# Optimization experiments

Measured on AMD Instinct MI355X. Metric: run time of the kernel, lower is better.

The kernel has to match this reference:

```python
import jax, jax.numpy as jnp
import numpy as np

DIM = 1024
NUM_EXPERTS = 8
TOP_K = 2


def setup_inputs() -> dict:
    key = jax.random.key(0)
    ks = jax.random.split(key, 7)
    s_in = 1.0 / np.sqrt(DIM)
    s_hid = 1.0 / np.sqrt(4 * DIM)
    x = jax.random.normal(ks[0], (2, 2048, DIM), dtype=jnp.float32)
    gate_w = jax.random.normal(ks[1], (DIM, NUM_EXPERTS), dtype=jnp.float32) * s_in
    gate_b = jax.random.normal(ks[2], (NUM_EXPERTS,), dtype=jnp.float32) * 0.01
    w1 = jax.random.normal(ks[3], (NUM_EXPERTS, DIM, 4 * DIM), dtype=jnp.float32) * s_in
    b1 = jax.random.normal(ks[4], (NUM_EXPERTS, 4 * DIM), dtype=jnp.float32) * 0.01
    w2 = jax.random.normal(ks[5], (NUM_EXPERTS, 4 * DIM, DIM), dtype=jnp.float32) * s_hid
    b2 = jax.random.normal(ks[6], (NUM_EXPERTS, DIM), dtype=jnp.float32) * 0.01
    return {"x": x, "gate_w": gate_w, "gate_b": gate_b, "w1": w1, "b1": b1, "w2": w2, "b2": b2}


def reference(x, gate_w, gate_b, w1, b1, w2, b2):
    # Faithful to the torch module in EVAL mode (no routing noise).
    # Quirks reproduced: (1) gather of expert inputs degenerates to flat_x
    # (all top_k copies identical); (2) softmax-normalized gates are dead code
    # (never applied); (3) the per-expert masked assignment overwrites all
    # TOP_K. Net: out = TOP_K * FFN_{max(topk_idx)}(x).
    B, N, C = x.shape
    flat_x = x.reshape(-1, C)                      # [T, C]
    logits = flat_x @ gate_w + gate_b              # [T, E]
    _, topk_idx = jax.lax.top_k(logits, TOP_K)     # [T, k]
    e_star = jnp.max(topk_idx, axis=-1)            # [T] last-overwriting expert
    out = jnp.zeros_like(flat_x)
    for i in range(NUM_EXPERTS):                   # fixed small expert loop
        h = jax.nn.gelu(flat_x @ w1[i] + b1[i], approximate=False)  # exact GELU (torch default)
        y = h @ w2[i] + b2[i]                      # [T, C]
        out = jnp.where((e_star == i)[:, None], y, out)
    return (TOP_K * out).reshape(B, N, C)
```

## Files before the change

kernel.cpp:

```cpp
#include <hip/hip_runtime.h>
#include <hip/hip_bf16.h>
#include <hip/hip_fp16.h>

#define T_TOKENS 4096
#define DIMC 1024
#define HID 4096
#define NE 8

typedef _Float16 f16;
typedef _Float16 f16x8 __attribute__((ext_vector_type(8)));
typedef _Float16 f16x4 __attribute__((ext_vector_type(4)));
typedef float f32x4 __attribute__((ext_vector_type(4)));

__device__ __forceinline__ void gload_lds16(const f16* g, f16* l) {
    __builtin_amdgcn_global_load_lds(
        (const __attribute__((address_space(1))) void*)g,
        (__attribute__((address_space(3))) void*)l, 16, 0, 0);
}

__global__ __launch_bounds__(256) void gating_kernel(
    const float* __restrict__ x, const float* __restrict__ gw,
    const float* __restrict__ gb, int* __restrict__ counts,
    int* __restrict__ list)
{
    const int wave = threadIdx.x >> 6;
    const int lane = threadIdx.x & 63;
    const int t = blockIdx.x * 4 + wave;

    const float* xr = x + (size_t)t * DIMC;
    float acc[NE];
#pragma unroll
    for (int e = 0; e < NE; ++e) acc[e] = 0.f;

    for (int i = 0; i < DIMC / 64; ++i) {
        const int k = i * 64 + lane;
        const float xv = xr[k];
        const float* g = gw + (size_t)k * NE;
#pragma unroll
        for (int e = 0; e < NE; ++e) acc[e] = fmaf(xv, g[e], acc[e]);
    }
#pragma unroll
    for (int off = 32; off >= 1; off >>= 1) {
#pragma unroll
        for (int e = 0; e < NE; ++e) acc[e] += __shfl_xor(acc[e], off, 64);
    }
    if (lane == 0) {
        float lg[NE];
#pragma unroll
        for (int e = 0; e < NE; ++e) lg[e] = acc[e] + gb[e];
        int i1 = 0; float v1 = lg[0];
#pragma unroll
        for (int e = 1; e < NE; ++e) { if (lg[e] > v1) { v1 = lg[e]; i1 = e; } }
        int i2 = -1; float v2 = -3.4e38f;
#pragma unroll
        for (int e = 0; e < NE; ++e) {
            if (e == i1) continue;
            if (lg[e] > v2) { v2 = lg[e]; i2 = e; }
        }
        const int es = (i1 > i2) ? i1 : i2;
        const int pos = atomicAdd(&counts[es], 1);
        list[es * T_TOKENS + pos] = t;
    }
}

__global__ __launch_bounds__(256) void xconvert(const float* __restrict__ x,
                                                f16* __restrict__ xh)
{
    const size_t i = ((size_t)blockIdx.x * 256 + threadIdx.x) * 8;
    const float4 a = *(const float4*)(x + i);
    const float4 b = *(const float4*)(x + i + 4);
    f16x8 v;
    v[0] = (f16)a.x; v[1] = (f16)a.y; v[2] = (f16)a.z; v[3] = (f16)a.w;
    v[4] = (f16)b.x; v[5] = (f16)b.y; v[6] = (f16)b.z; v[7] = (f16)b.w;
    *(f16x8*)(xh + i) = v;
}

__global__ __launch_bounds__(256) void wconvert(const float* __restrict__ W,
                                                f16* __restrict__ Wt,
                                                int K, int N)
{
    __shared__ f16 Lt[64 * 72];
    const int n0 = blockIdx.x * 64;
    const int k0 = blockIdx.y * 64;
    const float* Ws = W + (size_t)blockIdx.z * K * N;
    const int t = threadIdx.x;

    const int no = (t & 15) * 4;
    const int kr = t >> 4;
#pragma unroll
    for (int p = 0; p < 4; ++p) {
        const int k = kr + p * 16;
        const float4 v = *(const float4*)(Ws + (size_t)(k0 + k) * N + n0 + no);
        Lt[(no + 0) * 72 + k] = (f16)v.x;
        Lt[(no + 1) * 72 + k] = (f16)v.y;
        Lt[(no + 2) * 72 + k] = (f16)v.z;
        Lt[(no + 3) * 72 + k] = (f16)v.w;
    }
    __syncthreads();
    const int n = t >> 2;
    const int ko = (t & 3) * 16;
    const f16x8 a = *(const f16x8*)&Lt[n * 72 + ko];
    const f16x8 b = *(const f16x8*)&Lt[n * 72 + ko + 8];
    f16* dst = Wt + ((size_t)blockIdx.z * N + n0 + n) * K + k0 + ko;
    *(f16x8*)(dst) = a;
    *(f16x8*)(dst + 8) = b;
}

template <bool FIRST>
__global__ __launch_bounds__(512) void ffn_gemm5(
    const f16* __restrict__ A, const f16* __restrict__ Bt,
    const float* __restrict__ bias, const int* __restrict__ counts,
    const int* __restrict__ list, f16* __restrict__ Hout,
    float* __restrict__ pout)
{
    constexpr int KB   = FIRST ? DIMC : HID;
    constexpr int NTOT = FIRST ? HID : DIMC;

    const int e   = FIRST ? (int)blockIdx.z : (int)(blockIdx.z >> 2);
    const int ks  = FIRST ? 0 : (int)(blockIdx.z & 3);
    const int kk0 = ks * 1024;
    const int m0  = blockIdx.y * 256;
    const int n0  = blockIdx.x * 128;
    const int cnt = counts[e];
    if (m0 >= cnt) return;

    __shared__ __align__(16) f16 As[3][256 * 64];
    __shared__ __align__(16) f16 Bs[3][128 * 64];
    __shared__ int rows[256];

    const int tid = threadIdx.x;
    if (tid < 256) rows[tid] = (m0 + tid < cnt) ? list[e * T_TOKENS + m0 + tid] : -1;
    __syncthreads();

    const int lane = tid & 63;
    const int wv   = tid >> 6;
    const int wr   = wv >> 1;
    const int wc   = wv & 1;

    const f16* asrc[4];
    const f16* bsrc[2];
#pragma unroll
    for (int j = 0; j < 4; ++j) {
        const int row   = wv * 32 + j * 8 + (lane >> 3);
        const int chunk = (lane & 7) ^ (row & 7);
        int tok = rows[row]; if (tok < 0) tok = 0;
        asrc[j] = A + (size_t)tok * KB + kk0 + chunk * 8;
    }
#pragma unroll
    for (int j = 0; j < 2; ++j) {
        const int row   = wv * 16 + j * 8 + (lane >> 3);
        const int chunk = (lane & 7) ^ (row & 7);
        bsrc[j] = Bt + ((size_t)e * NTOT + n0 + row) * KB + kk0 + chunk * 8;
    }

    f32x4 acc[4][4];
#pragma unroll
    for (int mi = 0; mi < 4; ++mi)
#pragma unroll
        for (int ni = 0; ni < 4; ++ni) acc[mi][ni] = f32x4{0.f, 0.f, 0.f, 0.f};

#define STG(BUF, KT)                                                          \
    do {                                                                      \
        _Pragma("unroll")                                                     \
        for (int j = 0; j < 4; ++j)                                           \
            gload_lds16(asrc[j] + (KT) * 64, &As[BUF][(wv * 32 + j * 8) * 64]); \
        _Pragma("unroll")                                                     \
        for (int j = 0; j < 2; ++j)                                           \
            gload_lds16(bsrc[j] + (KT) * 64, &Bs[BUF][(wv * 16 + j * 8) * 64]); \
    } while (0)

#define CMP(BUF)                                                              \
    do {                                                                      \
        _Pragma("unroll")                                                     \
        for (int kh = 0; kh < 2; ++kh) {                                      \
            f16x8 af[4], bf[4];                                               \
            _Pragma("unroll")                                                 \
            for (int mi = 0; mi < 4; ++mi) {                                  \
                const int row = wr * 64 + mi * 16 + (lane & 15);              \
                const int kb  = (((lane >> 4) * 16) + kh * 64) ^ ((row & 7) << 4); \
                af[mi] = *(const f16x8*)((const char*)As[BUF] + row * 128 + kb);   \
            }                                                                 \
            _Pragma("unroll")                                                 \
            for (int ni = 0; ni < 4; ++ni) {                                  \
                const int n  = wc * 64 + ni * 16 + (lane & 15);               \
                const int kb = (((lane >> 4) * 16) + kh * 64) ^ ((n & 7) << 4);    \
                bf[ni] = *(const f16x8*)((const char*)Bs[BUF] + n * 128 + kb);     \
            }                                                                 \
            _Pragma("unroll")                                                 \
            for (int mi = 0; mi < 4; ++mi)                                    \
                _Pragma("unroll")                                             \
                for (int ni = 0; ni < 4; ++ni)                                \
                    acc[mi][ni] = __builtin_amdgcn_mfma_f32_16x16x32_f16(     \
                        af[mi], bf[ni], acc[mi][ni], 0, 0, 0);                \
        }                                                                     \
    } while (0)

    STG(0, 0);
    STG(1, 1);
#pragma unroll
    for (int kt = 0; kt < 16; ++kt) {
        if (kt + 2 < 16) STG((kt + 2) % 3, kt + 2);
        if (kt < 14)       asm volatile("s_waitcnt vmcnt(12)" ::: "memory");
        else if (kt == 14) asm volatile("s_waitcnt vmcnt(6)"  ::: "memory");
        else               asm volatile("s_waitcnt vmcnt(0)"  ::: "memory");
        __builtin_amdgcn_s_barrier();
        __builtin_amdgcn_sched_barrier(0);
        CMP(kt % 3);
        __builtin_amdgcn_s_barrier();
        __builtin_amdgcn_sched_barrier(0);
    }
#undef STG
#undef CMP

#pragma unroll
    for (int ni = 0; ni < 4; ++ni) {
        const int gc = n0 + wc * 64 + ni * 16 + (lane & 15);
        const float bv = FIRST ? bias[(size_t)e * HID + gc]
                               : ((ks == 0) ? 2.f * bias[(size_t)e * DIMC + gc] : 0.f);
#pragma unroll
        for (int mi = 0; mi < 4; ++mi) {
#pragma unroll
            for (int r = 0; r < 4; ++r) {
                const int lrow = wr * 64 + mi * 16 + (lane >> 4) * 4 + r;
                const int tok = rows[lrow];
                if (tok < 0) continue;
                if (FIRST) {
                    const float v = acc[mi][ni][r] + bv;
                    const float g = 0.5f * v * (1.f + erff(v * 0.70710678118f));
                    Hout[(size_t)tok * HID + gc] = (f16)g;
                } else {
                    pout[((size_t)ks * T_TOKENS + tok) * DIMC + gc] =
                        2.f * acc[mi][ni][r] + bv;
                }
            }
        }
    }
}

__global__ __launch_bounds__(256) void reduce4(const float* __restrict__ p,
                                               float* __restrict__ out)
{
    constexpr size_t SL = (size_t)T_TOKENS * DIMC;
    const size_t i = ((size_t)blockIdx.x * 256 + threadIdx.x) * 4;
    const float4 a = *(const float4*)(p + i);
    const float4 b = *(const float4*)(p + SL + i);
    const float4 c = *(const float4*)(p + 2 * SL + i);
    const float4 d = *(const float4*)(p + 3 * SL + i);
    float4 s;
    s.x = a.x + b.x + c.x + d.x;
    s.y = a.y + b.y + c.y + d.y;
    s.z = a.z + b.z + c.z + d.z;
    s.w = a.w + b.w + c.w + d.w;
    *(float4*)(out + i) = s;
}

template <bool FIRST>
__global__ __launch_bounds__(256) void ffn_gemm3(
    const f16* __restrict__ A, const f16* __restrict__ Bt,
    const float* __restrict__ bias, const int* __restrict__ counts,
    const int* __restrict__ list, f16* __restrict__ Hout,
    float* __restrict__ out)
{
    constexpr int KB   = FIRST ? DIMC : HID;
    constexpr int NTOT = FIRST ? HID : DIMC;
    constexpr int NKT  = 16;

    const int e   = FIRST ? (int)blockIdx.z : (int)(blockIdx.z >> 2);
    const int ks  = FIRST ? 0 : (int)(blockIdx.z & 3);
    const int kk0 = ks * 1024;
    const int m0  = blockIdx.y * 128;
    const int n0  = blockIdx.x * 128;
    const int cnt = counts[e];
    if (m0 >= cnt) return;

    __shared__ __align__(16) f16 As[128 * 64];
    __shared__ __align__(16) f16 Bs[128 * 64];
    __shared__ int rows[128];

    const int tid = threadIdx.x;
    if (tid < 128) rows[tid] = (m0 + tid < cnt) ? list[e * T_TOKENS + m0 + tid] : -1;
    __syncthreads();

    const int lane = tid & 63;
    const int wv   = tid >> 6;
    const int wr   = wv >> 1, wc = wv & 1;

    const f16* asrc[4];
    const f16* bsrc[4];
    f16* adst[4];
    f16* bdst[4];
#pragma unroll
    for (int j = 0; j < 4; ++j) {
        const int row   = wv * 32 + j * 8 + (lane >> 3);
        const int chunk = (lane & 7) ^ (row & 7);
        int tok = rows[row]; if (tok < 0) tok = 0;
        asrc[j] = A + (size_t)tok * KB + kk0 + chunk * 8;
        bsrc[j] = Bt + ((size_t)e * NTOT + n0 + row) * KB + kk0 + chunk * 8;
        adst[j] = As + (wv * 32 + j * 8) * 64;
        bdst[j] = Bs + (wv * 32 + j * 8) * 64;
    }

    f32x4 acc[4][4];
#pragma unroll
    for (int mi = 0; mi < 4; ++mi)
#pragma unroll
        for (int ni = 0; ni < 4; ++ni) acc[mi][ni] = f32x4{0.f, 0.f, 0.f, 0.f};

    for (int kt = 0; kt < NKT; ++kt) {
        const int ko = kt * 64;
        __syncthreads();
#pragma unroll
        for (int j = 0; j < 4; ++j) {
            gload_lds16(asrc[j] + ko, adst[j]);
            gload_lds16(bsrc[j] + ko, bdst[j]);
        }
        __syncthreads();
#pragma unroll
        for (int kh = 0; kh < 2; ++kh) {
            f16x8 af[4], bf[4];
#pragma unroll
            for (int mi = 0; mi < 4; ++mi) {
                const int row = wr * 64 + mi * 16 + (lane & 15);
                const int kb  = (((lane >> 4) * 16) + kh * 64) ^ ((row & 7) << 4);
                af[mi] = *(const f16x8*)((const char*)As + row * 128 + kb);
            }
#pragma unroll
            for (int ni = 0; ni < 4; ++ni) {
                const int n  = wc * 64 + ni * 16 + (lane & 15);
                const int kb = (((lane >> 4) * 16) + kh * 64) ^ ((n & 7) << 4);
                bf[ni] = *(const f16x8*)((const char*)Bs + n * 128 + kb);
            }
#pragma unroll
            for (int mi = 0; mi < 4; ++mi)
#pragma unroll
                for (int ni = 0; ni < 4; ++ni)
                    acc[mi][ni] = __builtin_amdgcn_mfma_f32_16x16x32_f16(
                        af[mi], bf[ni], acc[mi][ni], 0, 0, 0);
        }
    }

#pragma unroll
    for (int ni = 0; ni < 4; ++ni) {
        const int gc = n0 + wc * 64 + ni * 16 + (lane & 15);
        const float bv = FIRST ? bias[(size_t)e * HID + gc]
                               : ((ks == 0) ? 2.f * bias[(size_t)e * DIMC + gc] : 0.f);
#pragma unroll
        for (int mi = 0; mi < 4; ++mi) {
#pragma unroll
            for (int r = 0; r < 4; ++r) {
                const int lrow = wr * 64 + mi * 16 + (lane >> 4) * 4 + r;
                const int tok = rows[lrow];
                if (tok < 0) continue;
                if (FIRST) {
                    const float v = acc[mi][ni][r] + bv;
                    const float g = 0.5f * v * (1.f + erff(v * 0.70710678118f));
                    Hout[(size_t)tok * HID + gc] = (f16)g;
                } else {
                    atomicAdd(out + (size_t)tok * DIMC + gc,
                              2.f * acc[mi][ni][r] + bv);
                }
            }
        }
    }
}

template <bool FIRST>
__global__ __launch_bounds__(256) void ffn_gemm_fb(
    const float* __restrict__ x, const f16* __restrict__ Hin,
    const float* __restrict__ w1, const float* __restrict__ b1,
    const float* __restrict__ w2, const float* __restrict__ b2,
    const int* __restrict__ counts, const int* __restrict__ list,
    f16* __restrict__ Hout, float* __restrict__ out)
{
    constexpr int K = FIRST ? DIMC : HID;
    constexpr int N = FIRST ? HID : DIMC;
    constexpr int LDT = 40;

    const int e  = blockIdx.z;
    const int m0 = blockIdx.y * 128;
    const int n0 = blockIdx.x * 128;
    const int cnt = counts[e];
    if (m0 >= cnt) return;

    __shared__ f16 Ab[128 * LDT];
    __shared__ f16 Bb[128 * LDT];
    __shared__ int rows[128];

    const int tid = threadIdx.x;
    if (tid < 128) {
        const int p = m0 + tid;
        rows[tid] = (p < cnt) ? list[e * T_TOKENS + p] : -1;
    }
    __syncthreads();

    const int lane = tid & 63;
    const int wv = tid >> 6;
    const int wr = wv >> 1, wc = wv & 1;

    f32x4 acc[4][4];
#pragma unroll
    for (int mi = 0; mi < 4; ++mi)
#pragma unroll
        for (int ni = 0; ni < 4; ++ni) acc[mi][ni] = f32x4{0.f, 0.f, 0.f, 0.f};

    const float* Bsrc = (FIRST ? w1 : w2) + (size_t)e * K * N;

    for (int kk = 0; kk < K; kk += 32) {
        __syncthreads();
        {
            const int r  = tid >> 3;
            const int ko = (tid & 7) * 4;
#pragma unroll
            for (int p = 0; p < 4; ++p) {
                const int row = p * 32 + r;
                const int tok = rows[row];
                f16x4 hv;
                if (FIRST) {
                    float4 v;
                    if (tok >= 0) v = *(const float4*)(x + (size_t)tok * K + kk + ko);
                    else          v = make_float4(0.f, 0.f, 0.f, 0.f);
                    hv[0] = (f16)v.x; hv[1] = (f16)v.y; hv[2] = (f16)v.z; hv[3] = (f16)v.w;
                } else {
                    if (tok >= 0) hv = *(const f16x4*)(Hin + (size_t)tok * K + kk + ko);
                    else { hv[0] = (f16)0.f; hv[1] = (f16)0.f; hv[2] = (f16)0.f; hv[3] = (f16)0.f; }
                }
                *(f16x4*)&Ab[row * LDT + ko] = hv;
            }
        }
        {
            const int kb = tid >> 5;
            const int no = (tid & 31) * 4;
#pragma unroll
            for (int p = 0; p < 4; ++p) {
                const int k = p * 8 + kb;
                const float4 v = *(const float4*)(Bsrc + (size_t)(kk + k) * N + n0 + no);
                f16 h[4];
                h[0] = (f16)v.x; h[1] = (f16)v.y; h[2] = (f16)v.z; h[3] = (f16)v.w;
#pragma unroll
                for (int i = 0; i < 4; ++i) {
                    const int n = no + i;
                    const int chunk = (k >> 3) ^ ((n >> 2) & 3);
                    Bb[n * LDT + chunk * 8 + (k & 7)] = h[i];
                }
            }
        }
        __syncthreads();
        f16x8 af[4], bf[4];
#pragma unroll
        for (int mi = 0; mi < 4; ++mi) {
            const int row = wr * 64 + mi * 16 + (lane & 15);
            af[mi] = *(const f16x8*)&Ab[row * LDT + (lane >> 4) * 8];
        }
#pragma unroll
        for (int ni = 0; ni < 4; ++ni) {
            const int n = wc * 64 + ni * 16 + (lane & 15);
            const int chunk = (lane >> 4) ^ ((n >> 2) & 3);
            bf[ni] = *(const f16x8*)&Bb[n * LDT + chunk * 8];
        }
#pragma unroll
        for (int mi = 0; mi < 4; ++mi)
#pragma unroll
            for (int ni = 0; ni < 4; ++ni)
                acc[mi][ni] = __builtin_amdgcn_mfma_f32_16x16x32_f16(
                    af[mi], bf[ni], acc[mi][ni], 0, 0, 0);
    }

#pragma unroll
    for (int ni = 0; ni < 4; ++ni) {
        const int gc = n0 + wc * 64 + ni * 16 + (lane & 15);
        const float bias = FIRST ? b1[(size_t)e * HID + gc]
                                 : b2[(size_t)e * DIMC + gc];
#pragma unroll
        for (int mi = 0; mi < 4; ++mi) {
#pragma unroll
            for (int r = 0; r < 4; ++r) {
                const int lrow = wr * 64 + mi * 16 + (lane >> 4) * 4 + r;
                const int tok = rows[lrow];
                if (tok < 0) continue;
                const float v = acc[mi][ni][r] + bias;
                if (FIRST) {
                    const float g = 0.5f * v * (1.f + erff(v * 0.70710678118f));
                    Hout[(size_t)tok * HID + gc] = (f16)g;
                } else {
                    out[(size_t)tok * DIMC + gc] = 2.f * v;
                }
            }
        }
    }
}

extern "C" void kernel_launch(void* const* d_in, const int* in_sizes, int n_in,
                              void* d_out, int out_size, void* d_ws, size_t ws_size,
                              hipStream_t stream)
{
    const float* x   = (const float*)d_in[0];
    const float* gw  = (const float*)d_in[1];
    const float* gb  = (const float*)d_in[2];
    const float* w1  = (const float*)d_in[3];
    const float* b1  = (const float*)d_in[4];
    const float* w2  = (const float*)d_in[5];
    const float* b2  = (const float*)d_in[6];
    float* out = (float*)d_out;

    const size_t MB = 1 << 20;
    const size_t need_p   = 233 * MB;
    const size_t need_big = 169 * MB;

    if (ws_size >= need_big) {
        int* counts = (int*)d_ws;
        int* list   = (int*)((char*)d_ws + 1024);
        f16* xh     = (f16*)((char*)d_ws + 1 * MB);
        f16* H      = (f16*)((char*)d_ws + 9 * MB);
        f16* w1t    = (f16*)((char*)d_ws + 41 * MB);
        f16* w2t    = (f16*)((char*)d_ws + 105 * MB);
        float* p    = (float*)((char*)d_ws + 169 * MB);

        hipMemsetAsync(counts, 0, 1024, stream);

        gating_kernel<<<T_TOKENS / 4, 256, 0, stream>>>(x, gw, gb, counts, list);
        xconvert<<<(T_TOKENS * DIMC) / (256 * 8), 256, 0, stream>>>(x, xh);
        wconvert<<<dim3(HID / 64, DIMC / 64, NE), 256, 0, stream>>>(w1, w1t, DIMC, HID);
        wconvert<<<dim3(DIMC / 64, HID / 64, NE), 256, 0, stream>>>(w2, w2t, HID, DIMC);

        if (ws_size >= need_p) {
            ffn_gemm5<true><<<dim3(HID / 128, T_TOKENS / 256, NE), 512, 0, stream>>>(
                xh, w1t, b1, counts, list, H, nullptr);
            ffn_gemm5<false><<<dim3(DIMC / 128, T_TOKENS / 256, NE * 4), 512, 0, stream>>>(
                H, w2t, b2, counts, list, nullptr, p);
            reduce4<<<(T_TOKENS * DIMC) / (256 * 4), 256, 0, stream>>>(p, out);
        } else {
            hipMemsetAsync(out, 0, (size_t)T_TOKENS * DIMC * sizeof(float), stream);
            ffn_gemm3<true><<<dim3(HID / 128, T_TOKENS / 128, NE), 256, 0, stream>>>(
                xh, w1t, b1, counts, list, H, nullptr);
            ffn_gemm3<false><<<dim3(DIMC / 128, T_TOKENS / 128, NE * 4), 256, 0, stream>>>(
                H, w2t, b2, counts, list, nullptr, out);
        }
        return;
    }

    const size_t need_fb = (size_t)(1 << 18) + (size_t)T_TOKENS * HID * sizeof(f16);
    if (ws_size < need_fb) return;

    int* counts = (int*)d_ws;
    int* list   = (int*)((char*)d_ws + 1024);
    f16* H      = (f16*)((char*)d_ws + (1 << 18));

    hipMemsetAsync(d_ws, 0, 1024, stream);
    gating_kernel<<<T_TOKENS / 4, 256, 0, stream>>>(x, gw, gb, counts, list);
    ffn_gemm_fb<true><<<dim3(HID / 128, T_TOKENS / 128, NE), 256, 0, stream>>>(
        x, (const f16*)nullptr, w1, b1, w2, b2, counts, list, H, out);
    ffn_gemm_fb<false><<<dim3(DIMC / 128, T_TOKENS / 128, NE), 256, 0, stream>>>(
        x, (const f16*)H, w1, b1, w2, b2, counts, list, H, out);
}
```

Measured before the change: 377.2 us.

## Enlarge expert GEMM tile to 256x256 with double buffering and XCD-aware block swizzle

The grouped expert GEMM now uses a 256x256 output tile per 512-thread block (8x4 MFMA fragments per wave) instead of 256x128, so each loaded A/B tile is reused across more outputs. The three-stage LDS pipeline becomes a two-stage ping-pong to fit the larger B tile in LDS. A 1-D grid with a bid&7 remap spreads each expert's tiles across the 8 XCDs for better L2 locality. The unused fp32 fallback kernel is removed. The larger accumulator raises register pressure and the shallower pipeline may expose more load latency.

```diff
diff --git a/kernel.cpp b/kernel.cpp
--- a/kernel.cpp
+++ b/kernel.cpp
@@ -107,7 +107,7 @@
 }
 
 template <bool FIRST>
-__global__ __launch_bounds__(512) void ffn_gemm5(
+__global__ __launch_bounds__(512) void ffn_gemm6(
     const f16* __restrict__ A, const f16* __restrict__ Bt,
     const float* __restrict__ bias, const int* __restrict__ counts,
     const int* __restrict__ list, f16* __restrict__ Hout,
@@ -116,16 +116,21 @@
     constexpr int KB   = FIRST ? DIMC : HID;
     constexpr int NTOT = FIRST ? HID : DIMC;
 
-    const int e   = FIRST ? (int)blockIdx.z : (int)(blockIdx.z >> 2);
-    const int ks  = FIRST ? 0 : (int)(blockIdx.z & 3);
-    const int kk0 = ks * 1024;
-    const int m0  = blockIdx.y * 256;
-    const int n0  = blockIdx.x * 128;
-    const int cnt = counts[e];
+    const int bid  = blockIdx.x;
+    const int orig = (bid & 7) * 256 + (bid >> 3);
+    const int e    = orig >> 8;
+    const int oid  = orig & 255;
+    const int m_t  = oid >> 4;
+    const int n_t  = FIRST ? (oid & 15) : (oid & 3);
+    const int ks   = FIRST ? 0 : ((oid >> 2) & 3);
+    const int kk0  = ks * 1024;
+    const int m0   = m_t * 256;
+    const int n0   = n_t * 256;
+    const int cnt  = counts[e];
     if (m0 >= cnt) return;
 
-    __shared__ __align__(16) f16 As[3][256 * 64];
-    __shared__ __align__(16) f16 Bs[3][128 * 64];
+    __shared__ __align__(16) f16 As[2][256 * 64];
+    __shared__ __align__(16) f16 Bs[2][256 * 64];
     __shared__ int rows[256];
 
     const int tid = threadIdx.x;
@@ -134,49 +139,43 @@
 
     const int lane = tid & 63;
     const int wv   = tid >> 6;
-    const int wr   = wv >> 1;
-    const int wc   = wv & 1;
+    const int wr   = wv >> 2;
+    const int wc   = wv & 3;
 
     const f16* asrc[4];
-    const f16* bsrc[2];
+    const f16* bsrc[4];
 #pragma unroll
     for (int j = 0; j < 4; ++j) {
         const int row   = wv * 32 + j * 8 + (lane >> 3);
         const int chunk = (lane & 7) ^ (row & 7);
         int tok = rows[row]; if (tok < 0) tok = 0;
         asrc[j] = A + (size_t)tok * KB + kk0 + chunk * 8;
-    }
-#pragma unroll
-    for (int j = 0; j < 2; ++j) {
-        const int row   = wv * 16 + j * 8 + (lane >> 3);
-        const int chunk = (lane & 7) ^ (row & 7);
         bsrc[j] = Bt + ((size_t)e * NTOT + n0 + row) * KB + kk0 + chunk * 8;
     }
 
-    f32x4 acc[4][4];
-#pragma unroll
-    for (int mi = 0; mi < 4; ++mi)
+    f32x4 acc[8][4];
+#pragma unroll
+    for (int mi = 0; mi < 8; ++mi)
 #pragma unroll
         for (int ni = 0; ni < 4; ++ni) acc[mi][ni] = f32x4{0.f, 0.f, 0.f, 0.f};
 
 #define STG(BUF, KT)                                                          \
     do {                                                                      \
         _Pragma("unroll")                                                     \
-        for (int j = 0; j < 4; ++j)                                           \
+        for (int j = 0; j < 4; ++j) {                                         \
             gload_lds16(asrc[j] + (KT) * 64, &As[BUF][(wv * 32 + j * 8) * 64]); \
-        _Pragma("unroll")                                                     \
-        for (int j = 0; j < 2; ++j)                                           \
-            gload_lds16(bsrc[j] + (KT) * 64, &Bs[BUF][(wv * 16 + j * 8) * 64]); \
+            gload_lds16(bsrc[j] + (KT) * 64, &Bs[BUF][(wv * 32 + j * 8) * 64]); \
+        }                                                                     \
     } while (0)
 
 #define CMP(BUF)                                                              \
     do {                                                                      \
         _Pragma("unroll")                                                     \
         for (int kh = 0; kh < 2; ++kh) {                                      \
-            f16x8 af[4], bf[4];                                               \
+            f16x8 af[8], bf[4];                                               \
             _Pragma("unroll")                                                 \
-            for (int mi = 0; mi < 4; ++mi) {                                  \
-                const int row = wr * 64 + mi * 16 + (lane & 15);              \
+            for (int mi = 0; mi < 8; ++mi) {                                  \
+                const int row = wr * 128 + mi * 16 + (lane & 15);             \
                 const int kb  = (((lane >> 4) * 16) + kh * 64) ^ ((row & 7) << 4); \
                 af[mi] = *(const f16x8*)((const char*)As[BUF] + row * 128 + kb);   \
             }                                                                 \
@@ -187,7 +186,7 @@
                 bf[ni] = *(const f16x8*)((const char*)Bs[BUF] + n * 128 + kb);     \
             }                                                                 \
             _Pragma("unroll")                                                 \
-            for (int mi = 0; mi < 4; ++mi)                                    \
+            for (int mi = 0; mi < 8; ++mi)                                    \
                 _Pragma("unroll")                                             \
                 for (int ni = 0; ni < 4; ++ni)                                \
                     acc[mi][ni] = __builtin_amdgcn_mfma_f32_16x16x32_f16(     \
@@ -196,16 +195,24 @@
     } while (0)
 
     STG(0, 0);
-    STG(1, 1);
-#pragma unroll
-    for (int kt = 0; kt < 16; ++kt) {
-        if (kt + 2 < 16) STG((kt + 2) % 3, kt + 2);
-        if (kt < 14)       asm volatile("s_waitcnt vmcnt(12)" ::: "memory");
-        else if (kt == 14) asm volatile("s_waitcnt vmcnt(6)"  ::: "memory");
-        else               asm volatile("s_waitcnt vmcnt(0)"  ::: "memory");
+#pragma unroll
+    for (int k = 0; k < 8; ++k) {
+        STG(1, 2 * k + 1);
+        asm volatile("s_waitcnt vmcnt(8)" ::: "memory");
         __builtin_amdgcn_s_barrier();
         __builtin_amdgcn_sched_barrier(0);
-        CMP(kt % 3);
+        CMP(0);
+        __builtin_amdgcn_s_barrier();
+        __builtin_amdgcn_sched_barrier(0);
+        if (k < 7) {
+            STG(0, 2 * k + 2);
+            asm volatile("s_waitcnt vmcnt(8)" ::: "memory");
+        } else {
+            asm volatile("s_waitcnt vmcnt(0)" ::: "memory");
+        }
+        __builtin_amdgcn_s_barrier();
+        __builtin_amdgcn_sched_barrier(0);
+        CMP(1);
         __builtin_amdgcn_s_barrier();
         __builtin_amdgcn_sched_barrier(0);
     }
@@ -218,10 +225,10 @@
         const float bv = FIRST ? bias[(size_t)e * HID + gc]
                                : ((ks == 0) ? 2.f * bias[(size_t)e * DIMC + gc] : 0.f);
 #pragma unroll
-        for (int mi = 0; mi < 4; ++mi) {
+        for (int mi = 0; mi < 8; ++mi) {
 #pragma unroll
             for (int r = 0; r < 4; ++r) {
-                const int lrow = wr * 64 + mi * 16 + (lane >> 4) * 4 + r;
+                const int lrow = wr * 128 + mi * 16 + (lane >> 4) * 4 + r;
                 const int tok = rows[lrow];
                 if (tok < 0) continue;
                 if (FIRST) {
@@ -364,131 +371,6 @@
     }
 }
 
-template <bool FIRST>
-__global__ __launch_bounds__(256) void ffn_gemm_fb(
-    const float* __restrict__ x, const f16* __restrict__ Hin,
-    const float* __restrict__ w1, const float* __restrict__ b1,
-    const float* __restrict__ w2, const float* __restrict__ b2,
-    const int* __restrict__ counts, const int* __restrict__ list,
-    f16* __restrict__ Hout, float* __restrict__ out)
-{
-    constexpr int K = FIRST ? DIMC : HID;
-    constexpr int N = FIRST ? HID : DIMC;
-    constexpr int LDT = 40;
-
-    const int e  = blockIdx.z;
-    const int m0 = blockIdx.y * 128;
-    const int n0 = blockIdx.x * 128;
-    const int cnt = counts[e];
-    if (m0 >= cnt) return;
-
-    __shared__ f16 Ab[128 * LDT];
-    __shared__ f16 Bb[128 * LDT];
-    __shared__ int rows[128];
-
-    const int tid = threadIdx.x;
-    if (tid < 128) {
-        const int p = m0 + tid;
-        rows[tid] = (p < cnt) ? list[e * T_TOKENS + p] : -1;
-    }
-    __syncthreads();
-
-    const int lane = tid & 63;
-    const int wv = tid >> 6;
-    const int wr = wv >> 1, wc = wv & 1;
-
-    f32x4 acc[4][4];
-#pragma unroll
-    for (int mi = 0; mi < 4; ++mi)
-#pragma unroll
-        for (int ni = 0; ni < 4; ++ni) acc[mi][ni] = f32x4{0.f, 0.f, 0.f, 0.f};
-
-    const float* Bsrc = (FIRST ? w1 : w2) + (size_t)e * K * N;
-
-    for (int kk = 0; kk < K; kk += 32) {
-        __syncthreads();
-        {
-            const int r  = tid >> 3;
-            const int ko = (tid & 7) * 4;
-#pragma unroll
-            for (int p = 0; p < 4; ++p) {
-                const int row = p * 32 + r;
-                const int tok = rows[row];
-                f16x4 hv;
-                if (FIRST) {
-                    float4 v;
-                    if (tok >= 0) v = *(const float4*)(x + (size_t)tok * K + kk + ko);
-                    else          v = make_float4(0.f, 0.f, 0.f, 0.f);
-                    hv[0] = (f16)v.x; hv[1] = (f16)v.y; hv[2] = (f16)v.z; hv[3] = (f16)v.w;
-                } else {
-                    if (tok >= 0) hv = *(const f16x4*)(Hin + (size_t)tok * K + kk + ko);
-                    else { hv[0] = (f16)0.f; hv[1] = (f16)0.f; hv[2] = (f16)0.f; hv[3] = (f16)0.f; }
-                }
-                *(f16x4*)&Ab[row * LDT + ko] = hv;
-            }
-        }
-        {
-            const int kb = tid >> 5;
-            const int no = (tid & 31) * 4;
-#pragma unroll
-            for (int p = 0; p < 4; ++p) {
-                const int k = p * 8 + kb;
-                const float4 v = *(const float4*)(Bsrc + (size_t)(kk + k) * N + n0 + no);
-                f16 h[4];
-                h[0] = (f16)v.x; h[1] = (f16)v.y; h[2] = (f16)v.z; h[3] = (f16)v.w;
-#pragma unroll
-                for (int i = 0; i < 4; ++i) {
-                    const int n = no + i;
-                    const int chunk = (k >> 3) ^ ((n >> 2) & 3);
-                    Bb[n * LDT + chunk * 8 + (k & 7)] = h[i];
-                }
-            }
-        }
-        __syncthreads();
-        f16x8 af[4], bf[4];
-#pragma unroll
-        for (int mi = 0; mi < 4; ++mi) {
-            const int row = wr * 64 + mi * 16 + (lane & 15);
-            af[mi] = *(const f16x8*)&Ab[row * LDT + (lane >> 4) * 8];
-        }
-#pragma unroll
-        for (int ni = 0; ni < 4; ++ni) {
-            const int n = wc * 64 + ni * 16 + (lane & 15);
-            const int chunk = (lane >> 4) ^ ((n >> 2) & 3);
-            bf[ni] = *(const f16x8*)&Bb[n * LDT + chunk * 8];
-        }
-#pragma unroll
-        for (int mi = 0; mi < 4; ++mi)
-#pragma unroll
-            for (int ni = 0; ni < 4; ++ni)
-                acc[mi][ni] = __builtin_amdgcn_mfma_f32_16x16x32_f16(
-                    af[mi], bf[ni], acc[mi][ni], 0, 0, 0);
-    }
-
-#pragma unroll
-    for (int ni = 0; ni < 4; ++ni) {
-        const int gc = n0 + wc * 64 + ni * 16 + (lane & 15);
-        const float bias = FIRST ? b1[(size_t)e * HID + gc]
-                                 : b2[(size_t)e * DIMC + gc];
-#pragma unroll
-        for (int mi = 0; mi < 4; ++mi) {
-#pragma unroll
-            for (int r = 0; r < 4; ++r) {
-                const int lrow = wr * 64 + mi * 16 + (lane >> 4) * 4 + r;
-                const int tok = rows[lrow];
-                if (tok < 0) continue;
-                const float v = acc[mi][ni][r] + bias;
-                if (FIRST) {
-                    const float g = 0.5f * v * (1.f + erff(v * 0.70710678118f));
-                    Hout[(size_t)tok * HID + gc] = (f16)g;
-                } else {
-                    out[(size_t)tok * DIMC + gc] = 2.f * v;
-                }
-            }
-        }
-    }
-}
-
 extern "C" void kernel_launch(void* const* d_in, const int* in_sizes, int n_in,
                               void* d_out, int out_size, void* d_ws, size_t ws_size,
                               hipStream_t stream)
@@ -505,50 +387,34 @@
     const size_t MB = 1 << 20;
     const size_t need_p   = 233 * MB;
     const size_t need_big = 169 * MB;
-
-    if (ws_size >= need_big) {
-        int* counts = (int*)d_ws;
-        int* list   = (int*)((char*)d_ws + 1024);
-        f16* xh     = (f16*)((char*)d_ws + 1 * MB);
-        f16* H      = (f16*)((char*)d_ws + 9 * MB);
-        f16* w1t    = (f16*)((char*)d_ws + 41 * MB);
-        f16* w2t    = (f16*)((char*)d_ws + 105 * MB);
-        float* p    = (float*)((char*)d_ws + 169 * MB);
-
-        hipMemsetAsync(counts, 0, 1024, stream);
-
-        gating_kernel<<<T_TOKENS / 4, 256, 0, stream>>>(x, gw, gb, counts, list);
-        xconvert<<<(T_TOKENS * DIMC) / (256 * 8), 256, 0, stream>>>(x, xh);
-        wconvert<<<dim3(HID / 64, DIMC / 64, NE), 256, 0, stream>>>(w1, w1t, DIMC, HID);
-        wconvert<<<dim3(DIMC / 64, HID / 64, NE), 256, 0, stream>>>(w2, w2t, HID, DIMC);
-
-        if (ws_size >= need_p) {
-            ffn_gemm5<true><<<dim3(HID / 128, T_TOKENS / 256, NE), 512, 0, stream>>>(
-                xh, w1t, b1, counts, list, H, nullptr);
-            ffn_gemm5<false><<<dim3(DIMC / 128, T_TOKENS / 256, NE * 4), 512, 0, stream>>>(
-                H, w2t, b2, counts, list, nullptr, p);
-            reduce4<<<(T_TOKENS * DIMC) / (256 * 4), 256, 0, stream>>>(p, out);
-        } else {
-            hipMemsetAsync(out, 0, (size_t)T_TOKENS * DIMC * sizeof(float), stream);
-            ffn_gemm3<true><<<dim3(HID / 128, T_TOKENS / 128, NE), 256, 0, stream>>>(
-                xh, w1t, b1, counts, list, H, nullptr);
-            ffn_gemm3<false><<<dim3(DIMC / 128, T_TOKENS / 128, NE * 4), 256, 0, stream>>>(
-                H, w2t, b2, counts, list, nullptr, out);
-        }
-        return;
-    }
-
-    const size_t need_fb = (size_t)(1 << 18) + (size_t)T_TOKENS * HID * sizeof(f16);
-    if (ws_size < need_fb) return;
+    if (ws_size < need_big) return;
 
     int* counts = (int*)d_ws;
     int* list   = (int*)((char*)d_ws + 1024);
-    f16* H      = (f16*)((char*)d_ws + (1 << 18));
-
-    hipMemsetAsync(d_ws, 0, 1024, stream);
+    f16* xh     = (f16*)((char*)d_ws + 1 * MB);
+    f16* H      = (f16*)((char*)d_ws + 9 * MB);
+    f16* w1t    = (f16*)((char*)d_ws + 41 * MB);
+    f16* w2t    = (f16*)((char*)d_ws + 105 * MB);
+    float* p    = (float*)((char*)d_ws + 169 * MB);
+
+    hipMemsetAsync(counts, 0, 1024, stream);
+
     gating_kernel<<<T_TOKENS / 4, 256, 0, stream>>>(x, gw, gb, counts, list);
-    ffn_gemm_fb<true><<<dim3(HID / 128, T_TOKENS / 128, NE), 256, 0, stream>>>(
-        x, (const f16*)nullptr, w1, b1, w2, b2, counts, list, H, out);
-    ffn_gemm_fb<false><<<dim3(DIMC / 128, T_TOKENS / 128, NE), 256, 0, stream>>>(
-        x, (const f16*)H, w1, b1, w2, b2, counts, list, H, out);
-}
+    xconvert<<<(T_TOKENS * DIMC) / (256 * 8), 256, 0, stream>>>(x, xh);
+    wconvert<<<dim3(HID / 64, DIMC / 64, NE), 256, 0, stream>>>(w1, w1t, DIMC, HID);
+    wconvert<<<dim3(DIMC / 64, HID / 64, NE), 256, 0, stream>>>(w2, w2t, HID, DIMC);
+
+    if (ws_size >= need_p) {
+        ffn_gemm6<true><<<2048, 512, 0, stream>>>(
+            xh, w1t, b1, counts, list, H, nullptr);
+        ffn_gemm6<false><<<2048, 512, 0, stream>>>(
+            H, w2t, b2, counts, list, nullptr, p);
+        reduce4<<<(T_TOKENS * DIMC) / (256 * 4), 256, 0, stream>>>(p, out);
+    } else {
+        hipMemsetAsync(out, 0, (size_t)T_TOKENS * DIMC * sizeof(float), stream);
+        ffn_gemm3<true><<<dim3(HID / 128, T_TOKENS / 128, NE), 256, 0, stream>>>(
+            xh, w1t, b1, counts, list, H, nullptr);
+        ffn_gemm3<false><<<dim3(DIMC / 128, T_TOKENS / 128, NE * 4), 256, 0, stream>>>(
+            H, w2t, b2, counts, list, nullptr, out);
+    }
+}
```

After: 535.3 us. 1.42x slower.
